# Kernel optimization log

Measured on AMD Instinct MI355X. Metric: run time of the kernel, lower is better.

The kernel has to match this reference:

```python
import jax, jax.numpy as jnp
import numpy as np

D_K = 64
NEG = -1.0e9

def setup_inputs() -> dict:
    key = jax.random.key(0)
    k1, k2, k3 = jax.random.split(key, 3)
    B, S, Dk = 4, 4096, D_K
    query = jax.random.normal(k1, (B, S, Dk), dtype=jnp.float32)
    key_t = jax.random.normal(k2, (B, S, Dk), dtype=jnp.float32)
    value = jax.random.normal(k3, (B, S, Dk), dtype=jnp.float32)
    # causal mask: 1 = attend, 0 = blocked (broadcast over batch)
    mask = jnp.broadcast_to(jnp.tril(jnp.ones((S, S), dtype=jnp.int32)), (B, S, S))
    return {"query": query, "key": key_t, "value": value, "mask": mask}

def reference(query, key, value, mask):
    # scores = Q K^T / sqrt(d_k)  -> [B, S, S]
    scores = jnp.einsum("bqd,bkd->bqk", query, key) / jnp.sqrt(jnp.float32(D_K))
    scores = jnp.where(mask == 0, jnp.float32(NEG), scores)
    attention_weights = jax.nn.softmax(scores, axis=-1)
    # dropout p=0 (eval mode) -> identity
    output = jnp.einsum("bqk,bkd->bqd", attention_weights, value)
    return (output, attention_weights)
```

## Files before the change

kernel.cpp:

```cpp
#include <hip/hip_runtime.h>
#include <math.h>


constexpr int B_ = 4;
constexpr int S_ = 4096;
constexpr int DK_ = 64;
constexpr int NT = 256;
constexpr int NSP1 = 16;
constexpr int NSP = 8;
constexpr float SCALE = 0.125f;
constexpr float MBASE = 16.0f;

typedef __attribute__((ext_vector_type(8))) short bf16x8;
typedef __attribute__((ext_vector_type(4))) float f32x4;

__device__ __forceinline__ ushort f2bf(float x) {
  union { float f; unsigned u; } v; v.f = x;
  unsigned r = v.u + 0x7FFFu + ((v.u >> 16) & 1u);
  return (ushort)(r >> 16);
}
__device__ __forceinline__ float bf2f(ushort h) {
  union { float f; unsigned u; } v; v.u = ((unsigned)h) << 16;
  return v.f;
}

__global__ __launch_bounds__(256) void prep_all(
    const float* __restrict__ Q, const float* __restrict__ K,
    const float* __restrict__ V, ushort* __restrict__ Qh,
    ushort* __restrict__ Ql, ushort* __restrict__ Kb,
    ushort* __restrict__ Vt) {
  const int bx = blockIdx.x;
  const int tid = threadIdx.x;
  if (bx < 256) {
    __shared__ ushort t_s[64][72];
    const int b = bx >> 6;
    const int s0 = (bx & 63) * 64;
    const float* Vb = V + (size_t)b * S_ * DK_;
    ushort* VTb = Vt + (size_t)b * DK_ * S_;
#pragma unroll
    for (int it = 0; it < 4; ++it) {
      int idx = tid + it * 256;
      int sl = idx >> 4, dc = (idx & 15) << 2;
      float4 v = *reinterpret_cast<const float4*>(Vb + (size_t)(s0 + sl) * DK_ + dc);
      t_s[dc + 0][sl] = f2bf(v.x);
      t_s[dc + 1][sl] = f2bf(v.y);
      t_s[dc + 2][sl] = f2bf(v.z);
      t_s[dc + 3][sl] = f2bf(v.w);
    }
    __syncthreads();
#pragma unroll
    for (int it = 0; it < 2; ++it) {
      int idx = tid + it * 256;
      int d = idx >> 3, ch = (idx & 7) << 3;
      ushort tmp[8];
#pragma unroll
      for (int e = 0; e < 8; ++e) tmp[e] = t_s[d][ch + e];
      *reinterpret_cast<bf16x8*>(VTb + (size_t)d * S_ + s0 + ch) =
          *reinterpret_cast<const bf16x8*>(tmp);
    }
  } else {
    const int n4 = (B_ * S_ * DK_) / 4;
    int i = (bx - 256) * 256 + tid;
    const int stride = 512 * 256;
    for (; i < 2 * n4; i += stride) {
      if (i < n4) {
        float4 x = reinterpret_cast<const float4*>(Q)[i];
        ushort4 h, l;
        h.x = f2bf(x.x); l.x = f2bf(x.x - bf2f(h.x));
        h.y = f2bf(x.y); l.y = f2bf(x.y - bf2f(h.y));
        h.z = f2bf(x.z); l.z = f2bf(x.z - bf2f(h.z));
        h.w = f2bf(x.w); l.w = f2bf(x.w - bf2f(h.w));
        reinterpret_cast<ushort4*>(Qh)[i] = h;
        reinterpret_cast<ushort4*>(Ql)[i] = l;
      } else {
        int j = i - n4;
        float4 x = reinterpret_cast<const float4*>(K)[j];
        ushort4 h;
        h.x = f2bf(x.x); h.y = f2bf(x.y); h.z = f2bf(x.z); h.w = f2bf(x.w);
        reinterpret_cast<ushort4*>(Kb)[j] = h;
      }
    }
  }
}

__global__ __launch_bounds__(NT) void part_l(
    const ushort* __restrict__ Qh, const ushort* __restrict__ Ql,
    const ushort* __restrict__ Kb, float* __restrict__ Ml) {
  const int qt = blockIdx.x;
  const int sp = blockIdx.y;
  const int b = blockIdx.z;
  const int kts = sp * 4;
  if (kts > qt) return;
  const int kte = min(kts + 4, qt + 1);

  __shared__ __align__(16) ushort k_s[64 * 64];

  const int q0 = qt * 64;
  const int tid = threadIdx.x;
  const int wave = tid >> 6;
  const int lane = tid & 63;
  const int lg = lane >> 4;
  const int lc = lane & 15;

  const ushort* Qhb = Qh + (size_t)b * S_ * DK_;
  const ushort* Qlb = Ql + (size_t)b * S_ * DK_;
  const ushort* Kbb = Kb + (size_t)b * S_ * DK_;

  const int qw0 = q0 + wave * 16;

  bf16x8 qh[2], ql[2];
#pragma unroll
  for (int kk = 0; kk < 2; ++kk) {
    size_t off = (size_t)(qw0 + lc) * DK_ + kk * 32 + lg * 8;
    qh[kk] = *reinterpret_cast<const bf16x8*>(Qhb + off);
    ql[kk] = *reinterpret_cast<const bf16x8*>(Qlb + off);
  }

  float l_r[4] = {0.f, 0.f, 0.f, 0.f};

  for (int kt = kts; kt < kte; ++kt) {
    const int kv0 = kt * 64;
    __syncthreads();
#pragma unroll
    for (int i = 0; i < 2; ++i) {
      int idx = tid + i * NT;
      int r = idx >> 3, c = idx & 7;
      int dst = r * 64 + ((c * 8) ^ ((r & 7) << 3));
      *reinterpret_cast<bf16x8*>(&k_s[dst]) =
          *reinterpret_cast<const bf16x8*>(Kbb + (size_t)(kv0 + r) * DK_ + c * 8);
    }
    __syncthreads();

    f32x4 s[4];
#pragma unroll
    for (int n = 0; n < 4; ++n) {
      const int kvl = n * 16 + lc;
      const int sw = (kvl & 7) << 3;
      f32x4 acc = {0.f, 0.f, 0.f, 0.f};
#pragma unroll
      for (int kk = 0; kk < 2; ++kk) {
        bf16x8 kb = *reinterpret_cast<const bf16x8*>(
            &k_s[kvl * 64 + ((kk * 32 + lg * 8) ^ sw)]);
        acc = __builtin_amdgcn_mfma_f32_16x16x32_bf16(qh[kk], kb, acc, 0, 0, 0);
        acc = __builtin_amdgcn_mfma_f32_16x16x32_bf16(ql[kk], kb, acc, 0, 0, 0);
      }
      s[n] = acc;
    }

#pragma unroll
    for (int r = 0; r < 4; ++r) {
      const int qg = qw0 + lg * 4 + r;
#pragma unroll
      for (int n = 0; n < 4; ++n) {
        int kvg = kv0 + n * 16 + lc;
        float e = (kvg <= qg) ? __expf(s[n][r] * SCALE - MBASE) : 0.f;
        l_r[r] += e;
      }
    }
  }

#pragma unroll
  for (int r = 0; r < 4; ++r) {
    float l = l_r[r];
    l += __shfl_xor(l, 1);
    l += __shfl_xor(l, 2);
    l += __shfl_xor(l, 4);
    l += __shfl_xor(l, 8);
    if (lc == 0)
      Ml[((size_t)(b * 64 + qt) * NSP1 + sp) * 64 + wave * 16 + lg * 4 + r] = l;
  }
}

__global__ __launch_bounds__(NT) void attn_out(
    const ushort* __restrict__ Qh, const ushort* __restrict__ Ql,
    const ushort* __restrict__ Kb, const ushort* __restrict__ Vt,
    const float* __restrict__ Ml, float* __restrict__ Wg,
    float* __restrict__ Opart) {
  const int qt = blockIdx.x;
  const int sp = blockIdx.y;
  const int b = blockIdx.z;
  const int kts = sp * 8;
  const int kte = min(kts + 8, qt + 1);
  const int q0 = qt * 64;
  const int tid = threadIdx.x;

  float* Wb = Wg + (size_t)b * S_ * S_;

  {
    const int zr = tid >> 4;
    const int zc = (tid & 15) << 2;
    const float4 z = make_float4(0.f, 0.f, 0.f, 0.f);
    for (int kt = max(kts, qt + 1); kt < kts + 8; ++kt) {
#pragma unroll
      for (int e = 0; e < 4; ++e) {
        int row = zr + e * 16;
        *reinterpret_cast<float4*>(Wb + (size_t)(q0 + row) * S_ + kt * 64 + zc) = z;
      }
    }
  }
  if (kts > qt) return;

  __shared__ __align__(16) ushort k_s[64 * 64];
  __shared__ __align__(16) ushort v_s[64 * 64];
  __shared__ __align__(16) ushort w_s[64 * 64];
  __shared__ float il_f[64];

  const int wave = tid >> 6;
  const int lane = tid & 63;
  const int lg = lane >> 4;
  const int lc = lane & 15;
  const int nact1 = qt / 4 + 1;

  if (tid < 64) {
    const float* src = Ml + (size_t)(b * 64 + qt) * NSP1 * 64 + tid;
    float l = 0.f;
#pragma unroll
    for (int s_ = 0; s_ < NSP1; ++s_)
      l += (s_ < nact1) ? src[s_ * 64] : 0.f;
    il_f[tid] = 1.0f / l;
  }

  const ushort* Qhb = Qh + (size_t)b * S_ * DK_;
  const ushort* Qlb = Ql + (size_t)b * S_ * DK_;
  const ushort* Kbb = Kb + (size_t)b * S_ * DK_;
  const ushort* Vtb = Vt + (size_t)b * DK_ * S_;

  const int qw0 = q0 + wave * 16;

  bf16x8 qh[2], ql[2];
#pragma unroll
  for (int kk = 0; kk < 2; ++kk) {
    size_t off = (size_t)(qw0 + lc) * DK_ + kk * 32 + lg * 8;
    qh[kk] = *reinterpret_cast<const bf16x8*>(Qhb + off);
    ql[kk] = *reinterpret_cast<const bf16x8*>(Qlb + off);
  }

  __syncthreads();
  float il_r[4];
#pragma unroll
  for (int r = 0; r < 4; ++r) il_r[r] = il_f[wave * 16 + lg * 4 + r];

  f32x4 o_acc[4];
#pragma unroll
  for (int n = 0; n < 4; ++n) o_acc[n] = (f32x4){0.f, 0.f, 0.f, 0.f};

  for (int kt = kts; kt < kte; ++kt) {
    const int kv0 = kt * 64;
    __syncthreads();
#pragma unroll
    for (int i = 0; i < 2; ++i) {
      int idx = tid + i * NT;
      int r = idx >> 3, c = idx & 7;
      int dst = r * 64 + ((c * 8) ^ ((r & 7) << 3));
      *reinterpret_cast<bf16x8*>(&k_s[dst]) =
          *reinterpret_cast<const bf16x8*>(Kbb + (size_t)(kv0 + r) * DK_ + c * 8);
      *reinterpret_cast<bf16x8*>(&v_s[dst]) =
          *reinterpret_cast<const bf16x8*>(Vtb + (size_t)r * S_ + kv0 + c * 8);
    }
    __syncthreads();

    f32x4 s[4];
#pragma unroll
    for (int n = 0; n < 4; ++n) {
      const int kvl = n * 16 + lc;
      const int sw = (kvl & 7) << 3;
      f32x4 acc = {0.f, 0.f, 0.f, 0.f};
#pragma unroll
      for (int kk = 0; kk < 2; ++kk) {
        bf16x8 kb = *reinterpret_cast<const bf16x8*>(
            &k_s[kvl * 64 + ((kk * 32 + lg * 8) ^ sw)]);
        acc = __builtin_amdgcn_mfma_f32_16x16x32_bf16(qh[kk], kb, acc, 0, 0, 0);
        acc = __builtin_amdgcn_mfma_f32_16x16x32_bf16(ql[kk], kb, acc, 0, 0, 0);
      }
      s[n] = acc;
    }

#pragma unroll
    for (int r = 0; r < 4; ++r) {
      const int qg = qw0 + lg * 4 + r;
      const int qloc = wave * 16 + lg * 4 + r;
      const int qsw = (qloc & 7) << 3;
      const float il = il_r[r];
#pragma unroll
      for (int n = 0; n < 4; ++n) {
        int col = n * 16 + lc;
        int kvg = kv0 + col;
        float w = (kvg <= qg) ? __expf(s[n][r] * SCALE - MBASE) * il : 0.f;
        w_s[qloc * 64 + (col ^ qsw)] = f2bf(w);
      }
    }
    __syncthreads();

#pragma unroll
    for (int e = 0; e < 4; ++e) {
      const int row = (tid >> 4) + e * 16;
      const int pc = (tid & 15) << 2;
      ushort4 u = *reinterpret_cast<const ushort4*>(&w_s[row * 64 + pc]);
      float4 val = make_float4(bf2f(u.x), bf2f(u.y), bf2f(u.z), bf2f(u.w));
      const int lcol = pc ^ ((row & 7) << 3);
      *reinterpret_cast<float4*>(Wb + (size_t)(q0 + row) * S_ + kv0 + lcol) = val;
    }

    const int qrow = wave * 16 + lc;
    const int qrsw = (qrow & 7) << 3;
#pragma unroll
    for (int kk = 0; kk < 2; ++kk) {
      bf16x8 wa = *reinterpret_cast<const bf16x8*>(
          &w_s[qrow * 64 + ((kk * 32 + lg * 8) ^ qrsw)]);
#pragma unroll
      for (int n = 0; n < 4; ++n) {
        int drow = n * 16 + lc;
        bf16x8 vb = *reinterpret_cast<const bf16x8*>(
            &v_s[drow * 64 + ((kk * 32 + lg * 8) ^ ((drow & 7) << 3))]);
        o_acc[n] = __builtin_amdgcn_mfma_f32_16x16x32_bf16(wa, vb, o_acc[n], 0, 0, 0);
      }
    }
  }

  float* Op = Opart + ((size_t)((b * 64 + qt) * NSP + sp)) * (64 * 64);
#pragma unroll
  for (int r = 0; r < 4; ++r) {
    const int qr = wave * 16 + lg * 4 + r;
#pragma unroll
    for (int n = 0; n < 4; ++n)
      Op[(size_t)qr * 64 + n * 16 + lc] = o_acc[n][r];
  }
}

__global__ void reduce_o(const float* __restrict__ Opart, float* __restrict__ Og) {
  int i = blockIdx.x * blockDim.x + threadIdx.x;
  const int n4 = (B_ * S_ * DK_) / 4;
  const int stride = gridDim.x * blockDim.x;
  for (; i < n4; i += stride) {
    int e = i * 4;
    int rr = e >> 6;
    int dc = e & 63;
    int b = rr >> 12, q = rr & (S_ - 1);
    int qt = q >> 6, rl = q & 63;
    int nact = qt / 8 + 1;
    size_t base = ((size_t)((b * 64 + qt) * NSP)) * (64 * 64) + (size_t)rl * 64 + dc;
    float4 acc = make_float4(0.f, 0.f, 0.f, 0.f);
    for (int s_ = 0; s_ < nact; ++s_) {
      float4 p = *reinterpret_cast<const float4*>(Opart + base + (size_t)s_ * (64 * 64));
      acc.x += p.x; acc.y += p.y; acc.z += p.z; acc.w += p.w;
    }
    *reinterpret_cast<float4*>(Og + e) = acc;
  }
}

extern "C" void kernel_launch(void* const* d_in, const int* in_sizes, int n_in,
                              void* d_out, int out_size, void* d_ws, size_t ws_size,
                              hipStream_t stream) {
  const float* Q = (const float*)d_in[0];
  const float* K = (const float*)d_in[1];
  const float* V = (const float*)d_in[2];
  float* Og = (float*)d_out;
  float* Wg = Og + (size_t)B_ * S_ * DK_;

  const size_t NE = (size_t)B_ * S_ * DK_;
  ushort* Qh = (ushort*)d_ws;
  ushort* Ql = Qh + NE;
  ushort* Kb = Ql + NE;
  ushort* Vt = Kb + NE;
  float* Ml = (float*)(Vt + NE);
  float* Opart = Ml + (size_t)B_ * 64 * NSP1 * 64;

  prep_all<<<768, 256, 0, stream>>>(Q, K, V, Qh, Ql, Kb, Vt);

  dim3 grid1(S_ / 64, NSP1, B_);
  part_l<<<grid1, NT, 0, stream>>>(Qh, Ql, Kb, Ml);
  dim3 grid2(S_ / 64, NSP, B_);
  attn_out<<<grid2, NT, 0, stream>>>(Qh, Ql, Kb, Vt, Ml, Wg, Opart);
  reduce_o<<<256, 256, 0, stream>>>(Opart, Og);
}
```

Measured before the change: 108.4 us.

## Load K/V MFMA fragments directly from global memory and transpose score tiles

Drops the shared-memory staging of K and V tiles in both the row-sum and output kernels. MFMA fragments are now read straight from global memory (through the caches), which removes two block barriers per tile. The score MFMA operands are swapped so each lane holds four consecutive key columns for one query row. This lets the row sums finish with two shuffles, and the weights go to LDS as packed 4-element stores. Causal masking now applies only on the diagonal tile. The trade-off is possibly uncoalesced or redundant global loads of K and V across waves in exchange for fewer barriers and less LDS traffic.

```diff
diff --git a/kernel.cpp b/kernel.cpp
--- a/kernel.cpp
+++ b/kernel.cpp
@@ -93,9 +93,6 @@
   if (kts > qt) return;
   const int kte = min(kts + 4, qt + 1);
 
-  __shared__ __align__(16) ushort k_s[64 * 64];
-
-  const int q0 = qt * 64;
   const int tid = threadIdx.x;
   const int wave = tid >> 6;
   const int lane = tid & 63;
@@ -106,69 +103,54 @@
   const ushort* Qlb = Ql + (size_t)b * S_ * DK_;
   const ushort* Kbb = Kb + (size_t)b * S_ * DK_;
 
-  const int qw0 = q0 + wave * 16;
-
-  bf16x8 qh[2], ql[2];
+  const int qw0 = qt * 64 + wave * 16;
+
+  bf16x8 qh[2], qlr[2];
 #pragma unroll
   for (int kk = 0; kk < 2; ++kk) {
     size_t off = (size_t)(qw0 + lc) * DK_ + kk * 32 + lg * 8;
     qh[kk] = *reinterpret_cast<const bf16x8*>(Qhb + off);
-    ql[kk] = *reinterpret_cast<const bf16x8*>(Qlb + off);
-  }
-
-  float l_r[4] = {0.f, 0.f, 0.f, 0.f};
+    qlr[kk] = *reinterpret_cast<const bf16x8*>(Qlb + off);
+  }
+
+  const int qg = qw0 + lc;
+  float l = 0.f;
 
   for (int kt = kts; kt < kte; ++kt) {
     const int kv0 = kt * 64;
-    __syncthreads();
-#pragma unroll
-    for (int i = 0; i < 2; ++i) {
-      int idx = tid + i * NT;
-      int r = idx >> 3, c = idx & 7;
-      int dst = r * 64 + ((c * 8) ^ ((r & 7) << 3));
-      *reinterpret_cast<bf16x8*>(&k_s[dst]) =
-          *reinterpret_cast<const bf16x8*>(Kbb + (size_t)(kv0 + r) * DK_ + c * 8);
-    }
-    __syncthreads();
-
     f32x4 s[4];
 #pragma unroll
     for (int n = 0; n < 4; ++n) {
-      const int kvl = n * 16 + lc;
-      const int sw = (kvl & 7) << 3;
       f32x4 acc = {0.f, 0.f, 0.f, 0.f};
 #pragma unroll
       for (int kk = 0; kk < 2; ++kk) {
-        bf16x8 kb = *reinterpret_cast<const bf16x8*>(
-            &k_s[kvl * 64 + ((kk * 32 + lg * 8) ^ sw)]);
-        acc = __builtin_amdgcn_mfma_f32_16x16x32_bf16(qh[kk], kb, acc, 0, 0, 0);
-        acc = __builtin_amdgcn_mfma_f32_16x16x32_bf16(ql[kk], kb, acc, 0, 0, 0);
+        bf16x8 kf = *reinterpret_cast<const bf16x8*>(
+            Kbb + (size_t)(kv0 + n * 16 + lc) * DK_ + kk * 32 + lg * 8);
+        acc = __builtin_amdgcn_mfma_f32_16x16x32_bf16(kf, qh[kk], acc, 0, 0, 0);
+        acc = __builtin_amdgcn_mfma_f32_16x16x32_bf16(kf, qlr[kk], acc, 0, 0, 0);
       }
       s[n] = acc;
     }
-
-#pragma unroll
-    for (int r = 0; r < 4; ++r) {
-      const int qg = qw0 + lg * 4 + r;
-#pragma unroll
-      for (int n = 0; n < 4; ++n) {
-        int kvg = kv0 + n * 16 + lc;
-        float e = (kvg <= qg) ? __expf(s[n][r] * SCALE - MBASE) : 0.f;
-        l_r[r] += e;
-      }
-    }
-  }
-
-#pragma unroll
-  for (int r = 0; r < 4; ++r) {
-    float l = l_r[r];
-    l += __shfl_xor(l, 1);
-    l += __shfl_xor(l, 2);
-    l += __shfl_xor(l, 4);
-    l += __shfl_xor(l, 8);
-    if (lc == 0)
-      Ml[((size_t)(b * 64 + qt) * NSP1 + sp) * 64 + wave * 16 + lg * 4 + r] = l;
-  }
+    if (kt < qt) {
+#pragma unroll
+      for (int n = 0; n < 4; ++n)
+#pragma unroll
+        for (int r = 0; r < 4; ++r) l += __expf(s[n][r] * SCALE - MBASE);
+    } else {
+#pragma unroll
+      for (int n = 0; n < 4; ++n)
+#pragma unroll
+        for (int r = 0; r < 4; ++r) {
+          int kvg = kv0 + n * 16 + lg * 4 + r;
+          l += (kvg <= qg) ? __expf(s[n][r] * SCALE - MBASE) : 0.f;
+        }
+    }
+  }
+
+  l += __shfl_xor(l, 16);
+  l += __shfl_xor(l, 32);
+  if (lane < 16)
+    Ml[((size_t)(b * 64 + qt) * NSP1 + sp) * 64 + wave * 16 + lc] = l;
 }
 
 __global__ __launch_bounds__(NT) void attn_out(
@@ -200,8 +182,6 @@
   }
   if (kts > qt) return;
 
-  __shared__ __align__(16) ushort k_s[64 * 64];
-  __shared__ __align__(16) ushort v_s[64 * 64];
   __shared__ __align__(16) ushort w_s[64 * 64];
   __shared__ float il_f[64];
 
@@ -227,18 +207,19 @@
 
   const int qw0 = q0 + wave * 16;
 
-  bf16x8 qh[2], ql[2];
+  bf16x8 qh[2], qlr[2];
 #pragma unroll
   for (int kk = 0; kk < 2; ++kk) {
     size_t off = (size_t)(qw0 + lc) * DK_ + kk * 32 + lg * 8;
     qh[kk] = *reinterpret_cast<const bf16x8*>(Qhb + off);
-    ql[kk] = *reinterpret_cast<const bf16x8*>(Qlb + off);
+    qlr[kk] = *reinterpret_cast<const bf16x8*>(Qlb + off);
   }
 
   __syncthreads();
-  float il_r[4];
-#pragma unroll
-  for (int r = 0; r < 4; ++r) il_r[r] = il_f[wave * 16 + lg * 4 + r];
+  const int qg = qw0 + lc;
+  const int qloc = wave * 16 + lc;
+  const int qsw = (qloc & 7) << 3;
+  const float il = il_f[qloc];
 
   f32x4 o_acc[4];
 #pragma unroll
@@ -246,48 +227,41 @@
 
   for (int kt = kts; kt < kte; ++kt) {
     const int kv0 = kt * 64;
+
+    f32x4 s[4];
+#pragma unroll
+    for (int n = 0; n < 4; ++n) {
+      f32x4 acc = {0.f, 0.f, 0.f, 0.f};
+#pragma unroll
+      for (int kk = 0; kk < 2; ++kk) {
+        bf16x8 kf = *reinterpret_cast<const bf16x8*>(
+            Kbb + (size_t)(kv0 + n * 16 + lc) * DK_ + kk * 32 + lg * 8);
+        acc = __builtin_amdgcn_mfma_f32_16x16x32_bf16(kf, qh[kk], acc, 0, 0, 0);
+        acc = __builtin_amdgcn_mfma_f32_16x16x32_bf16(kf, qlr[kk], acc, 0, 0, 0);
+      }
+      s[n] = acc;
+    }
+
     __syncthreads();
-#pragma unroll
-    for (int i = 0; i < 2; ++i) {
-      int idx = tid + i * NT;
-      int r = idx >> 3, c = idx & 7;
-      int dst = r * 64 + ((c * 8) ^ ((r & 7) << 3));
-      *reinterpret_cast<bf16x8*>(&k_s[dst]) =
-          *reinterpret_cast<const bf16x8*>(Kbb + (size_t)(kv0 + r) * DK_ + c * 8);
-      *reinterpret_cast<bf16x8*>(&v_s[dst]) =
-          *reinterpret_cast<const bf16x8*>(Vtb + (size_t)r * S_ + kv0 + c * 8);
-    }
-    __syncthreads();
-
-    f32x4 s[4];
+
+    const bool diag = (kt == qt);
 #pragma unroll
     for (int n = 0; n < 4; ++n) {
-      const int kvl = n * 16 + lc;
-      const int sw = (kvl & 7) << 3;
-      f32x4 acc = {0.f, 0.f, 0.f, 0.f};
-#pragma unroll
-      for (int kk = 0; kk < 2; ++kk) {
-        bf16x8 kb = *reinterpret_cast<const bf16x8*>(
-            &k_s[kvl * 64 + ((kk * 32 + lg * 8) ^ sw)]);
-        acc = __builtin_amdgcn_mfma_f32_16x16x32_bf16(qh[kk], kb, acc, 0, 0, 0);
-        acc = __builtin_amdgcn_mfma_f32_16x16x32_bf16(ql[kk], kb, acc, 0, 0, 0);
-      }
-      s[n] = acc;
-    }
-
-#pragma unroll
-    for (int r = 0; r < 4; ++r) {
-      const int qg = qw0 + lg * 4 + r;
-      const int qloc = wave * 16 + lg * 4 + r;
-      const int qsw = (qloc & 7) << 3;
-      const float il = il_r[r];
-#pragma unroll
-      for (int n = 0; n < 4; ++n) {
-        int col = n * 16 + lc;
-        int kvg = kv0 + col;
-        float w = (kvg <= qg) ? __expf(s[n][r] * SCALE - MBASE) * il : 0.f;
-        w_s[qloc * 64 + (col ^ qsw)] = f2bf(w);
-      }
+      ushort4 pk;
+      float w0 = __expf(s[n][0] * SCALE - MBASE) * il;
+      float w1 = __expf(s[n][1] * SCALE - MBASE) * il;
+      float w2 = __expf(s[n][2] * SCALE - MBASE) * il;
+      float w3 = __expf(s[n][3] * SCALE - MBASE) * il;
+      if (diag) {
+        int kvb = kv0 + n * 16 + lg * 4;
+        w0 = (kvb + 0 <= qg) ? w0 : 0.f;
+        w1 = (kvb + 1 <= qg) ? w1 : 0.f;
+        w2 = (kvb + 2 <= qg) ? w2 : 0.f;
+        w3 = (kvb + 3 <= qg) ? w3 : 0.f;
+      }
+      pk.x = f2bf(w0); pk.y = f2bf(w1); pk.z = f2bf(w2); pk.w = f2bf(w3);
+      *reinterpret_cast<ushort4*>(
+          &w_s[qloc * 64 + ((n * 16 + lg * 4) ^ qsw)]) = pk;
     }
     __syncthreads();
 
@@ -301,17 +275,14 @@
       *reinterpret_cast<float4*>(Wb + (size_t)(q0 + row) * S_ + kv0 + lcol) = val;
     }
 
-    const int qrow = wave * 16 + lc;
-    const int qrsw = (qrow & 7) << 3;
 #pragma unroll
     for (int kk = 0; kk < 2; ++kk) {
       bf16x8 wa = *reinterpret_cast<const bf16x8*>(
-          &w_s[qrow * 64 + ((kk * 32 + lg * 8) ^ qrsw)]);
+          &w_s[qloc * 64 + ((kk * 32 + lg * 8) ^ qsw)]);
 #pragma unroll
       for (int n = 0; n < 4; ++n) {
-        int drow = n * 16 + lc;
         bf16x8 vb = *reinterpret_cast<const bf16x8*>(
-            &v_s[drow * 64 + ((kk * 32 + lg * 8) ^ ((drow & 7) << 3))]);
+            Vtb + (size_t)(n * 16 + lc) * S_ + kv0 + kk * 32 + lg * 8);
         o_acc[n] = __builtin_amdgcn_mfma_f32_16x16x32_bf16(wa, vb, o_acc[n], 0, 0, 0);
       }
     }
```

New measurement: 208.4 us. 1.92x slower.
